# Performance work log

Measured on AMD Instinct MI355X. Metric: run time of the kernel, lower is better.

Reference implementation:

```python
import jax, jax.numpy as jnp
import numpy as np

EPS = 1e-5
GROUPS = 128  # 4 bands * nearest_power_of_2_divisor(256, 32)

def _haar_bands(x):
    # x: (C, H, W), H and W even -> SAME pad is a no-op for 2x2 stride-2 conv.
    # lax conv is cross-correlation: band[i,j] = sum_ab x[2i+a, 2j+b] * k[a,b]
    C, H, W = x.shape
    xr = x.reshape(C, H // 2, 2, W // 2, 2)
    x00 = xr[:, :, 0, :, 0]; x01 = xr[:, :, 0, :, 1]
    x10 = xr[:, :, 1, :, 0]; x11 = xr[:, :, 1, :, 1]
    half = jnp.asarray(0.5, x.dtype)  # (1/sqrt2)^2
    LL = (x00 + x01 + x10 + x11) * half
    HL = (-x00 - x01 + x10 + x11) * half  # outer(h1, h0)
    LH = (-x00 + x01 - x10 + x11) * half  # outer(h0, h1)
    HH = (x00 - x01 - x10 + x11) * half   # outer(h1, h1)
    return LL, HL, LH, HH

def _group_norm(y, scale, bias, groups, eps=EPS):
    C, H, W = y.shape
    yg = y.reshape(groups, C // groups, H, W)
    mean = jnp.mean(yg, axis=(1, 2, 3), keepdims=True)
    var = jnp.mean(jnp.square(yg - mean), axis=(1, 2, 3), keepdims=True)
    yn = ((yg - mean) * jax.lax.rsqrt(var + eps)).reshape(C, H, W)
    return yn * scale[:, None, None] + bias[:, None, None]

def setup_inputs() -> dict:
    key = jax.random.key(0)
    k1, k2 = jax.random.split(key)
    C, H, W, Cout = 256, 256, 256, 512
    x = jax.random.normal(k1, (C, H, W), dtype=jnp.float32)
    gn_scale = jnp.ones((4 * C,), dtype=jnp.float32)
    gn_bias = jnp.zeros((4 * C,), dtype=jnp.float32)
    w_proj = jax.random.normal(k2, (Cout, 4 * C), dtype=jnp.float32) / np.sqrt(4 * C)
    return {"x": x, "gn_scale": gn_scale, "gn_bias": gn_bias, "w_proj": w_proj}

def reference(x, gn_scale, gn_bias, w_proj):
    LL, HL, LH, HH = _haar_bands(x)
    y = jnp.concatenate([LL, HL, LH, HH], axis=0)   # (4C, H/2, W/2)
    y = _group_norm(y, gn_scale, gn_bias, GROUPS)
    y = jnp.einsum('oc,chw->ohw', w_proj, y)        # 1x1 conv, no bias
    y = jax.nn.relu(y)
    # dropout p=0.0 / inference -> identity
    return y
```

## Files before the change

kernel.cpp:

```cpp
#include <hip/hip_runtime.h>
#include <stdint.h>

typedef float  f32x2 __attribute__((ext_vector_type(2)));
typedef float  f32x4 __attribute__((ext_vector_type(4)));
typedef short  s16x8 __attribute__((ext_vector_type(8)));
typedef unsigned short u16;

#define GN_EPS 1e-5f


__device__ __forceinline__ u16 f2bf(float f) {
  unsigned u = __float_as_uint(f);
  u += 0x7fffu + ((u >> 16) & 1u);
  return (u16)(u >> 16);
}

__device__ __forceinline__ float wave_red_sum(float v) {
#pragma unroll
  for (int off = 32; off > 0; off >>= 1) v += __shfl_down(v, off, 64);
  return v;
}

__device__ __forceinline__ void gload16(const void* g, void* l) {
  __builtin_amdgcn_global_load_lds(
      (const __attribute__((address_space(1))) uint32_t*)(uintptr_t)g,
      (__attribute__((address_space(3))) uint32_t*)(uintptr_t)l,
      16, 0, 0);
}

__global__ __launch_bounds__(256) void haar_kernel(
    const float* __restrict__ x, u16* __restrict__ yt,
    float* __restrict__ gsum, float* __restrict__ gsqs)
{
  const int t    = threadIdx.x;
  const int cti  = t & 7;
  const int hwi  = t >> 3;
  const int hw0  = blockIdx.x * 64 + hwi * 2;
  const int h    = hw0 >> 7, w = hw0 & 127;
  const int cin0 = blockIdx.y * 64 + cti * 8;

  float sv[4] = {0.f,0.f,0.f,0.f}, qv[4] = {0.f,0.f,0.f,0.f};
  s16x8 ov[2][4];

  const float* xb = x + ((size_t)cin0 << 16) + (size_t)(2*h)*256 + (size_t)(2*w);
#pragma unroll
  for (int j = 0; j < 8; ++j) {
    const float* xp = xb + ((size_t)j << 16);
    f32x4 r0 = *(const f32x4*)(xp);
    f32x4 r1 = *(const f32x4*)(xp + 256);
#pragma unroll
    for (int p = 0; p < 2; ++p) {
      float x00 = p ? r0.z : r0.x;
      float x01 = p ? r0.w : r0.y;
      float x10 = p ? r1.z : r1.x;
      float x11 = p ? r1.w : r1.y;
      float LL = 0.5f*( x00 + x01 + x10 + x11);
      float HL = 0.5f*(-x00 - x01 + x10 + x11);
      float LH = 0.5f*(-x00 + x01 - x10 + x11);
      float HH = 0.5f*( x00 - x01 - x10 + x11);
      ov[p][0][j] = (short)f2bf(LL);
      ov[p][1][j] = (short)f2bf(HL);
      ov[p][2][j] = (short)f2bf(LH);
      ov[p][3][j] = (short)f2bf(HH);
      sv[0] += LL; qv[0] += LL*LL;
      sv[1] += HL; qv[1] += HL*HL;
      sv[2] += LH; qv[2] += LH*LH;
      sv[3] += HH; qv[3] += HH*HH;
    }
  }

  u16* yb = yt + (size_t)hw0 * 1024 + cin0;
#pragma unroll
  for (int p = 0; p < 2; ++p)
#pragma unroll
    for (int b = 0; b < 4; ++b)
      *(s16x8*)(yb + p*1024 + b*256) = ov[p][b];

#pragma unroll
  for (int k = 0; k < 4; ++k) {
#pragma unroll
    for (int msk = 8; msk < 64; msk <<= 1) {
      sv[k] += __shfl_xor(sv[k], msk, 64);
      qv[k] += __shfl_xor(qv[k], msk, 64);
    }
  }
  __shared__ float red[4][8][8];
  const int lane = t & 63, wv = t >> 6;
  if (lane < 8) {
#pragma unroll
    for (int k = 0; k < 4; ++k) {
      red[wv][lane][k]     = sv[k];
      red[wv][lane][4 + k] = qv[k];
    }
  }
  __syncthreads();
  if (t < 64) {
    int c8 = t & 7, vi = t >> 3;
    float tot = red[0][c8][vi] + red[1][c8][vi] + red[2][c8][vi] + red[3][c8][vi];
    int b = vi & 3;
    int g = b*32 + blockIdx.y*8 + c8;
    if (vi < 4) atomicAdd(&gsum[g], tot);
    else        atomicAdd(&gsqs[g], tot);
  }
}

__global__ __launch_bounds__(256) void wprep_kernel(
    const float* __restrict__ wproj, const float* __restrict__ gsum,
    const float* __restrict__ gsqs, const float* __restrict__ scale,
    const float* __restrict__ bias, u16* __restrict__ wn, float* __restrict__ tvec)
{
  const int o = blockIdx.x;
  const int t = threadIdx.x;
  const float invN = 1.0f / 131072.0f;
  float acc = 0.f;
#pragma unroll
  for (int j = 0; j < 4; ++j) {
    int c = j*256 + t;
    int g = c >> 3;
    float mean = gsum[g] * invN;
    float var  = gsqs[g] * invN - mean * mean;
    float inv  = rsqrtf(var + GN_EPS);
    float a = scale[c] * inv;
    float b = bias[c] - mean * a;
    float wv = wproj[o*1024 + c];
    wn[o*1024 + c] = f2bf(wv * a);
    acc += wv * b;
  }
  acc = wave_red_sum(acc);
  __shared__ float red[4];
  int lane = t & 63, wvi = t >> 6;
  if (lane == 0) red[wvi] = acc;
  __syncthreads();
  if (t == 0) tvec[o] = red[0] + red[1] + red[2] + red[3];
}

#define BM 128
#define BN 128
#define BK 64

__global__ __launch_bounds__(256) void gemm_kernel(
    const u16* __restrict__ A,
    const u16* __restrict__ B,
    const float* __restrict__ tvec,
    float* __restrict__ out)
{
  __shared__ __align__(1024) u16 As[2][BM*BK];
  __shared__ __align__(1024) u16 Bs[2][BN*BK];

  const int tid  = threadIdx.x;
  const int lane = tid & 63, wave = tid >> 6;

  const int bid = blockIdx.x;
  const int cid = (bid & 7) * 64 + (bid >> 3);
  const int m0 = (cid & 3) * BM;
  const int n0 = (cid >> 2) * BN;

  const int wm = wave >> 1, wn_ = wave & 1;
  const int g = lane >> 4, r = lane & 15;

  f32x4 acc[4][4];
#pragma unroll
  for (int i = 0; i < 4; ++i)
#pragma unroll
    for (int j = 0; j < 4; ++j) acc[i][j] = (f32x4)(0.f);

  const int chunk0 = wave * 4;
  int srow[4], soff[4];
#pragma unroll
  for (int ci = 0; ci < 4; ++ci) {
    int linear = (chunk0 + ci) * 1024 + lane * 16;
    srow[ci] = linear >> 7;
    soff[ci] = (linear & 127) ^ ((srow[ci] & 7) << 4);
  }

  auto STAGE = [&](int buf, int k0) {
#pragma unroll
    for (int ci = 0; ci < 4; ++ci) {
      gload16((const char*)(A + (size_t)(m0 + srow[ci])*1024 + k0) + soff[ci],
              (char*)As[buf] + (chunk0 + ci)*1024);
      gload16((const char*)(B + (size_t)(n0 + srow[ci])*1024 + k0) + soff[ci],
              (char*)Bs[buf] + (chunk0 + ci)*1024);
    }
  };

  auto COMPUTE = [&](int buf) {
#pragma unroll
    for (int kk = 0; kk < 2; ++kk) {
      s16x8 av[4], bv[4];
      const int kb = g*16 + kk*64;
#pragma unroll
      for (int m = 0; m < 4; ++m) {
        int row = wm*64 + m*16 + r;
        av[m] = *(const s16x8*)((const char*)As[buf] + row*128 + (kb ^ ((row & 7) << 4)));
      }
#pragma unroll
      for (int n = 0; n < 4; ++n) {
        int row = wn_*64 + n*16 + r;
        bv[n] = *(const s16x8*)((const char*)Bs[buf] + row*128 + (kb ^ ((row & 7) << 4)));
      }
#pragma unroll
      for (int m = 0; m < 4; ++m)
#pragma unroll
        for (int n = 0; n < 4; ++n)
          acc[m][n] = __builtin_amdgcn_mfma_f32_16x16x32_bf16(av[m], bv[n], acc[m][n], 0, 0, 0);
    }
  };

  STAGE(0, 0);
  __syncthreads();
  int cur = 0;
#pragma unroll 1
  for (int t = 0; t < 15; ++t) {
    STAGE(cur ^ 1, (t + 1) * BK);
    COMPUTE(cur);
    __syncthreads();
    cur ^= 1;
  }
  COMPUTE(cur);

#pragma unroll
  for (int m = 0; m < 4; ++m) {
#pragma unroll
    for (int rr = 0; rr < 4; ++rr) {
      int o = m0 + wm*64 + m*16 + g*4 + rr;
      float tv = tvec[o];
      float* op = out + (size_t)o*16384 + n0 + wn_*64 + r;
#pragma unroll
      for (int n = 0; n < 4; ++n) {
        float v = acc[m][n][rr] + tv;
        op[n*16] = v > 0.f ? v : 0.f;
      }
    }
  }
}

extern "C" void kernel_launch(void* const* d_in, const int* in_sizes, int n_in,
                              void* d_out, int out_size, void* d_ws, size_t ws_size,
                              hipStream_t stream)
{
  const float* x  = (const float*)d_in[0];
  const float* sc = (const float*)d_in[1];
  const float* bi = (const float*)d_in[2];
  const float* wp = (const float*)d_in[3];
  float* out = (float*)d_out;

  char* ws = (char*)d_ws;
  float* gsum = (float*)(ws + 0);
  float* gsqs = (float*)(ws + 512);
  float* tv   = (float*)(ws + 9216);
  u16*   wn   = (u16*)(ws + 16384);
  u16*   yt   = (u16*)(ws + 2097152);

  hipMemsetAsync(ws, 0, 1024, stream);
  hipLaunchKernelGGL(haar_kernel,  dim3(256, 4), dim3(256), 0, stream, x, yt, gsum, gsqs);
  hipLaunchKernelGGL(wprep_kernel, dim3(512),    dim3(256), 0, stream, wp, gsum, gsqs, sc, bi, wn, tv);
  hipLaunchKernelGGL(gemm_kernel,  dim3(512),    dim3(256), 0, stream, wn, yt, tv, out);
}
```

Before: 138.7 us.

## Fuse haar, weight prep and GEMM into one cooperative kernel with grid syncs

Merges the three separate kernels into a single cooperative launch of 512 blocks. Each block handles two Haar tiles, then the blocks do a grid-wide sync, run the weight-normalization prep, sync again, and run the GEMM. The aim is to remove the launch overhead and inter-kernel gaps between the three launches. In exchange it adds two grid barriers. It also requires all 512 blocks to be co-resident, which pins occupancy at 2 blocks per CU with 64KB of LDS each. The Haar phase now runs with only 512 blocks instead of 1024.

```diff
diff --git a/kernel.cpp b/kernel.cpp
--- a/kernel.cpp
+++ b/kernel.cpp
@@ -1,7 +1,9 @@
 #include <hip/hip_runtime.h>
+#include <hip/hip_cooperative_groups.h>
 #include <stdint.h>
 
-typedef float  f32x2 __attribute__((ext_vector_type(2)));
+namespace cg = cooperative_groups;
+
 typedef float  f32x4 __attribute__((ext_vector_type(4)));
 typedef short  s16x8 __attribute__((ext_vector_type(8)));
 typedef unsigned short u16;
@@ -28,207 +30,208 @@
       16, 0, 0);
 }
 
-__global__ __launch_bounds__(256) void haar_kernel(
-    const float* __restrict__ x, u16* __restrict__ yt,
-    float* __restrict__ gsum, float* __restrict__ gsqs)
-{
-  const int t    = threadIdx.x;
-  const int cti  = t & 7;
-  const int hwi  = t >> 3;
-  const int hw0  = blockIdx.x * 64 + hwi * 2;
-  const int h    = hw0 >> 7, w = hw0 & 127;
-  const int cin0 = blockIdx.y * 64 + cti * 8;
-
-  float sv[4] = {0.f,0.f,0.f,0.f}, qv[4] = {0.f,0.f,0.f,0.f};
-  s16x8 ov[2][4];
-
-  const float* xb = x + ((size_t)cin0 << 16) + (size_t)(2*h)*256 + (size_t)(2*w);
-#pragma unroll
-  for (int j = 0; j < 8; ++j) {
-    const float* xp = xb + ((size_t)j << 16);
-    f32x4 r0 = *(const f32x4*)(xp);
-    f32x4 r1 = *(const f32x4*)(xp + 256);
-#pragma unroll
-    for (int p = 0; p < 2; ++p) {
-      float x00 = p ? r0.z : r0.x;
-      float x01 = p ? r0.w : r0.y;
-      float x10 = p ? r1.z : r1.x;
-      float x11 = p ? r1.w : r1.y;
-      float LL = 0.5f*( x00 + x01 + x10 + x11);
-      float HL = 0.5f*(-x00 - x01 + x10 + x11);
-      float LH = 0.5f*(-x00 + x01 - x10 + x11);
-      float HH = 0.5f*( x00 - x01 - x10 + x11);
-      ov[p][0][j] = (short)f2bf(LL);
-      ov[p][1][j] = (short)f2bf(HL);
-      ov[p][2][j] = (short)f2bf(LH);
-      ov[p][3][j] = (short)f2bf(HH);
-      sv[0] += LL; qv[0] += LL*LL;
-      sv[1] += HL; qv[1] += HL*HL;
-      sv[2] += LH; qv[2] += LH*LH;
-      sv[3] += HH; qv[3] += HH*HH;
-    }
-  }
-
-  u16* yb = yt + (size_t)hw0 * 1024 + cin0;
-#pragma unroll
-  for (int p = 0; p < 2; ++p)
-#pragma unroll
-    for (int b = 0; b < 4; ++b)
-      *(s16x8*)(yb + p*1024 + b*256) = ov[p][b];
-
-#pragma unroll
-  for (int k = 0; k < 4; ++k) {
-#pragma unroll
-    for (int msk = 8; msk < 64; msk <<= 1) {
-      sv[k] += __shfl_xor(sv[k], msk, 64);
-      qv[k] += __shfl_xor(qv[k], msk, 64);
-    }
-  }
-  __shared__ float red[4][8][8];
-  const int lane = t & 63, wv = t >> 6;
-  if (lane < 8) {
-#pragma unroll
-    for (int k = 0; k < 4; ++k) {
-      red[wv][lane][k]     = sv[k];
-      red[wv][lane][4 + k] = qv[k];
-    }
-  }
-  __syncthreads();
-  if (t < 64) {
-    int c8 = t & 7, vi = t >> 3;
-    float tot = red[0][c8][vi] + red[1][c8][vi] + red[2][c8][vi] + red[3][c8][vi];
-    int b = vi & 3;
-    int g = b*32 + blockIdx.y*8 + c8;
-    if (vi < 4) atomicAdd(&gsum[g], tot);
-    else        atomicAdd(&gsqs[g], tot);
-  }
-}
-
-__global__ __launch_bounds__(256) void wprep_kernel(
-    const float* __restrict__ wproj, const float* __restrict__ gsum,
-    const float* __restrict__ gsqs, const float* __restrict__ scale,
-    const float* __restrict__ bias, u16* __restrict__ wn, float* __restrict__ tvec)
-{
-  const int o = blockIdx.x;
-  const int t = threadIdx.x;
-  const float invN = 1.0f / 131072.0f;
-  float acc = 0.f;
-#pragma unroll
-  for (int j = 0; j < 4; ++j) {
-    int c = j*256 + t;
-    int g = c >> 3;
-    float mean = gsum[g] * invN;
-    float var  = gsqs[g] * invN - mean * mean;
-    float inv  = rsqrtf(var + GN_EPS);
-    float a = scale[c] * inv;
-    float b = bias[c] - mean * a;
-    float wv = wproj[o*1024 + c];
-    wn[o*1024 + c] = f2bf(wv * a);
-    acc += wv * b;
-  }
-  acc = wave_red_sum(acc);
-  __shared__ float red[4];
-  int lane = t & 63, wvi = t >> 6;
-  if (lane == 0) red[wvi] = acc;
-  __syncthreads();
-  if (t == 0) tvec[o] = red[0] + red[1] + red[2] + red[3];
-}
-
 #define BM 128
 #define BN 128
 #define BK 64
 
-__global__ __launch_bounds__(256) void gemm_kernel(
-    const u16* __restrict__ A,
-    const u16* __restrict__ B,
-    const float* __restrict__ tvec,
-    float* __restrict__ out)
+__global__ __launch_bounds__(256, 2) void fused_kernel(
+    const float* __restrict__ x, const float* __restrict__ scale,
+    const float* __restrict__ bias, const float* __restrict__ wproj,
+    u16* __restrict__ yt, float* __restrict__ gsum, float* __restrict__ gsqs,
+    u16* __restrict__ wn, float* __restrict__ tvec, float* __restrict__ out)
 {
   __shared__ __align__(1024) u16 As[2][BM*BK];
   __shared__ __align__(1024) u16 Bs[2][BN*BK];
+  __shared__ float redS[4][8][8];
 
   const int tid  = threadIdx.x;
+  const int bid  = blockIdx.x;
   const int lane = tid & 63, wave = tid >> 6;
 
-  const int bid = blockIdx.x;
-  const int cid = (bid & 7) * 64 + (bid >> 3);
-  const int m0 = (cid & 3) * BM;
-  const int n0 = (cid >> 2) * BN;
-
-  const int wm = wave >> 1, wn_ = wave & 1;
-  const int g = lane >> 4, r = lane & 15;
-
-  f32x4 acc[4][4];
-#pragma unroll
-  for (int i = 0; i < 4; ++i)
-#pragma unroll
-    for (int j = 0; j < 4; ++j) acc[i][j] = (f32x4)(0.f);
-
-  const int chunk0 = wave * 4;
-  int srow[4], soff[4];
-#pragma unroll
-  for (int ci = 0; ci < 4; ++ci) {
-    int linear = (chunk0 + ci) * 1024 + lane * 16;
-    srow[ci] = linear >> 7;
-    soff[ci] = (linear & 127) ^ ((srow[ci] & 7) << 4);
+#pragma unroll 1
+  for (int i = 0; i < 2; ++i) {
+    const int oid = bid * 2 + i;
+    const int bx  = oid & 255, by = oid >> 8;
+    const int cti = tid & 7;
+    const int hwi = tid >> 3;
+    const int hw0 = bx * 64 + hwi * 2;
+    const int h   = hw0 >> 7, w = hw0 & 127;
+    const int cin0 = by * 64 + cti * 8;
+
+    float sv[4] = {0.f,0.f,0.f,0.f}, qv[4] = {0.f,0.f,0.f,0.f};
+    s16x8 ov[2][4];
+
+    const float* xb = x + ((size_t)cin0 << 16) + (size_t)(2*h)*256 + (size_t)(2*w);
+#pragma unroll
+    for (int j = 0; j < 8; ++j) {
+      const float* xp = xb + ((size_t)j << 16);
+      f32x4 r0 = *(const f32x4*)(xp);
+      f32x4 r1 = *(const f32x4*)(xp + 256);
+#pragma unroll
+      for (int p = 0; p < 2; ++p) {
+        float x00 = p ? r0.z : r0.x;
+        float x01 = p ? r0.w : r0.y;
+        float x10 = p ? r1.z : r1.x;
+        float x11 = p ? r1.w : r1.y;
+        float LL = 0.5f*( x00 + x01 + x10 + x11);
+        float HL = 0.5f*(-x00 - x01 + x10 + x11);
+        float LH = 0.5f*(-x00 + x01 - x10 + x11);
+        float HH = 0.5f*( x00 - x01 - x10 + x11);
+        ov[p][0][j] = (short)f2bf(LL);
+        ov[p][1][j] = (short)f2bf(HL);
+        ov[p][2][j] = (short)f2bf(LH);
+        ov[p][3][j] = (short)f2bf(HH);
+        sv[0] += LL; qv[0] += LL*LL;
+        sv[1] += HL; qv[1] += HL*HL;
+        sv[2] += LH; qv[2] += LH*LH;
+        sv[3] += HH; qv[3] += HH*HH;
+      }
+    }
+
+    u16* yb = yt + (size_t)hw0 * 1024 + cin0;
+#pragma unroll
+    for (int p = 0; p < 2; ++p)
+#pragma unroll
+      for (int b = 0; b < 4; ++b)
+        *(s16x8*)(yb + p*1024 + b*256) = ov[p][b];
+
+#pragma unroll
+    for (int k = 0; k < 4; ++k) {
+#pragma unroll
+      for (int msk = 8; msk < 64; msk <<= 1) {
+        sv[k] += __shfl_xor(sv[k], msk, 64);
+        qv[k] += __shfl_xor(qv[k], msk, 64);
+      }
+    }
+    if (lane < 8) {
+#pragma unroll
+      for (int k = 0; k < 4; ++k) {
+        redS[wave][lane][k]     = sv[k];
+        redS[wave][lane][4 + k] = qv[k];
+      }
+    }
+    __syncthreads();
+    if (tid < 64) {
+      int c8 = tid & 7, vi = tid >> 3;
+      float tot = redS[0][c8][vi] + redS[1][c8][vi] + redS[2][c8][vi] + redS[3][c8][vi];
+      int b = vi & 3;
+      int g = b*32 + by*8 + c8;
+      if (vi < 4) atomicAdd(&gsum[g], tot);
+      else        atomicAdd(&gsqs[g], tot);
+    }
+    __syncthreads();
   }
 
-  auto STAGE = [&](int buf, int k0) {
+  __threadfence();
+  cg::this_grid().sync();
+
+  {
+    const int o = bid;
+    const float invN = 1.0f / 131072.0f;
+    float acc = 0.f;
+#pragma unroll
+    for (int j = 0; j < 4; ++j) {
+      int c = j*256 + tid;
+      int g = c >> 3;
+      float mean = gsum[g] * invN;
+      float var  = gsqs[g] * invN - mean * mean;
+      float inv  = rsqrtf(var + GN_EPS);
+      float a = scale[c] * inv;
+      float b = bias[c] - mean * a;
+      float wv = wproj[o*1024 + c];
+      wn[o*1024 + c] = f2bf(wv * a);
+      acc += wv * b;
+    }
+    acc = wave_red_sum(acc);
+    float* red = &redS[0][0][0];
+    if (lane == 0) red[wave] = acc;
+    __syncthreads();
+    if (tid == 0) tvec[o] = red[0] + red[1] + red[2] + red[3];
+  }
+
+  __threadfence();
+  cg::this_grid().sync();
+
+  {
+    const int cid = (bid & 7) * 64 + (bid >> 3);
+    const int m0 = (cid & 3) * BM;
+    const int n0 = (cid >> 2) * BN;
+
+    const int wm = wave >> 1, wn_ = wave & 1;
+    const int g = lane >> 4, r = lane & 15;
+
+    f32x4 acc[4][4];
+#pragma unroll
+    for (int i = 0; i < 4; ++i)
+#pragma unroll
+      for (int j = 0; j < 4; ++j) acc[i][j] = (f32x4)(0.f);
+
+    const int chunk0 = wave * 4;
+    int srow[4], soff[4];
 #pragma unroll
     for (int ci = 0; ci < 4; ++ci) {
-      gload16((const char*)(A + (size_t)(m0 + srow[ci])*1024 + k0) + soff[ci],
-              (char*)As[buf] + (chunk0 + ci)*1024);
-      gload16((const char*)(B + (size_t)(n0 + srow[ci])*1024 + k0) + soff[ci],
-              (char*)Bs[buf] + (chunk0 + ci)*1024);
-    }
-  };
-
-  auto COMPUTE = [&](int buf) {
-#pragma unroll
-    for (int kk = 0; kk < 2; ++kk) {
-      s16x8 av[4], bv[4];
-      const int kb = g*16 + kk*64;
-#pragma unroll
-      for (int m = 0; m < 4; ++m) {
-        int row = wm*64 + m*16 + r;
-        av[m] = *(const s16x8*)((const char*)As[buf] + row*128 + (kb ^ ((row & 7) << 4)));
-      }
-#pragma unroll
-      for (int n = 0; n < 4; ++n) {
-        int row = wn_*64 + n*16 + r;
-        bv[n] = *(const s16x8*)((const char*)Bs[buf] + row*128 + (kb ^ ((row & 7) << 4)));
-      }
-#pragma unroll
-      for (int m = 0; m < 4; ++m)
-#pragma unroll
-        for (int n = 0; n < 4; ++n)
-          acc[m][n] = __builtin_amdgcn_mfma_f32_16x16x32_bf16(av[m], bv[n], acc[m][n], 0, 0, 0);
-    }
-  };
-
-  STAGE(0, 0);
-  __syncthreads();
-  int cur = 0;
+      int linear = (chunk0 + ci) * 1024 + lane * 16;
+      srow[ci] = linear >> 7;
+      soff[ci] = (linear & 127) ^ ((srow[ci] & 7) << 4);
+    }
+
+    auto STAGE = [&](int buf, int k0) {
+#pragma unroll
+      for (int ci = 0; ci < 4; ++ci) {
+        gload16((const char*)(wn + (size_t)(m0 + srow[ci])*1024 + k0) + soff[ci],
+                (char*)As[buf] + (chunk0 + ci)*1024);
+        gload16((const char*)(yt + (size_t)(n0 + srow[ci])*1024 + k0) + soff[ci],
+                (char*)Bs[buf] + (chunk0 + ci)*1024);
+      }
+    };
+
+    auto COMPUTE = [&](int buf) {
+#pragma unroll
+      for (int kk = 0; kk < 2; ++kk) {
+        s16x8 av[4], bv[4];
+        const int kb = g*16 + kk*64;
+#pragma unroll
+        for (int m = 0; m < 4; ++m) {
+          int row = wm*64 + m*16 + r;
+          av[m] = *(const s16x8*)((const char*)As[buf] + row*128 + (kb ^ ((row & 7) << 4)));
+        }
+#pragma unroll
+        for (int n = 0; n < 4; ++n) {
+          int row = wn_*64 + n*16 + r;
+          bv[n] = *(const s16x8*)((const char*)Bs[buf] + row*128 + (kb ^ ((row & 7) << 4)));
+        }
+#pragma unroll
+        for (int m = 0; m < 4; ++m)
+#pragma unroll
+          for (int n = 0; n < 4; ++n)
+            acc[m][n] = __builtin_amdgcn_mfma_f32_16x16x32_bf16(av[m], bv[n], acc[m][n], 0, 0, 0);
+      }
+    };
+
+    STAGE(0, 0);
+    __syncthreads();
+    int cur = 0;
 #pragma unroll 1
-  for (int t = 0; t < 15; ++t) {
-    STAGE(cur ^ 1, (t + 1) * BK);
+    for (int kt = 0; kt < 15; ++kt) {
+      STAGE(cur ^ 1, (kt + 1) * BK);
+      COMPUTE(cur);
+      __syncthreads();
+      cur ^= 1;
+    }
     COMPUTE(cur);
-    __syncthreads();
-    cur ^= 1;
-  }
-  COMPUTE(cur);
-
-#pragma unroll
-  for (int m = 0; m < 4; ++m) {
-#pragma unroll
-    for (int rr = 0; rr < 4; ++rr) {
-      int o = m0 + wm*64 + m*16 + g*4 + rr;
-      float tv = tvec[o];
-      float* op = out + (size_t)o*16384 + n0 + wn_*64 + r;
-#pragma unroll
-      for (int n = 0; n < 4; ++n) {
-        float v = acc[m][n][rr] + tv;
-        op[n*16] = v > 0.f ? v : 0.f;
+
+#pragma unroll
+    for (int m = 0; m < 4; ++m) {
+#pragma unroll
+      for (int rr = 0; rr < 4; ++rr) {
+        int o = m0 + wm*64 + m*16 + g*4 + rr;
+        float tv = tvec[o];
+        float* op = out + (size_t)o*16384 + n0 + wn_*64 + r;
+#pragma unroll
+        for (int n = 0; n < 4; ++n) {
+          float v = acc[m][n][rr] + tv;
+          op[n*16] = v > 0.f ? v : 0.f;
+        }
       }
     }
   }
@@ -252,7 +255,10 @@
   u16*   yt   = (u16*)(ws + 2097152);
 
   hipMemsetAsync(ws, 0, 1024, stream);
-  hipLaunchKernelGGL(haar_kernel,  dim3(256, 4), dim3(256), 0, stream, x, yt, gsum, gsqs);
-  hipLaunchKernelGGL(wprep_kernel, dim3(512),    dim3(256), 0, stream, wp, gsum, gsqs, sc, bi, wn, tv);
-  hipLaunchKernelGGL(gemm_kernel,  dim3(512),    dim3(256), 0, stream, wn, yt, tv, out);
-}
+
+  void* args[] = {(void*)&x, (void*)&sc, (void*)&bi, (void*)&wp,
+                  (void*)&yt, (void*)&gsum, (void*)&gsqs,
+                  (void*)&wn, (void*)&tv, (void*)&out};
+  hipLaunchCooperativeKernel((const void*)fused_kernel, dim3(512), dim3(256),
+                             args, 0, stream);
+}
```

After: 371.4 us. +167.8%, slower.
